# Performance work log

Hardware: AMD Instinct MI355X
Metric: run time of the kernel (lower is better)

The kernel has to match this reference:

```python
import jax, jax.numpy as jnp
import numpy as np

H, D = 2, 32          # heads, per-head dim
F = H * D             # hidden_channels = 64
IN = 128              # raw input feature dim
N_PAPER, N_AUTHOR = 200000, 100000
E = 400000            # edges per edge type


def setup_inputs() -> dict:
    ks = iter(jax.random.split(jax.random.key(0), 64))
    def nrm(shape, scale=1.0):
        return jax.random.normal(next(ks), shape, dtype=jnp.float32) * scale
    def rint(n, hi):
        return jax.random.randint(next(ks), (n,), 0, hi, dtype=jnp.int32)
    s_in = float(1.0 / np.sqrt(IN)); s_f = float(1.0 / np.sqrt(F)); s_d = float(1.0 / np.sqrt(D))
    return dict(
        x_paper=nrm((N_PAPER, IN)), x_author=nrm((N_AUTHOR, IN)),
        ei_writes_src=rint(E, N_AUTHOR), ei_writes_dst=rint(E, N_PAPER),
        ei_cites_src=rint(E, N_PAPER), ei_cites_dst=rint(E, N_PAPER),
        ei_rev_src=rint(E, N_PAPER), ei_rev_dst=rint(E, N_AUTHOR),
        lin_W_paper=nrm((IN, F), s_in), lin_b_paper=jnp.zeros((F,), jnp.float32),
        lin_W_author=nrm((IN, F), s_in), lin_b_author=jnp.zeros((F,), jnp.float32),
        kqv_W_paper=nrm((F, 3 * F), s_f), kqv_b_paper=jnp.zeros((3 * F,), jnp.float32),
        kqv_W_author=nrm((F, 3 * F), s_f), kqv_b_author=jnp.zeros((3 * F,), jnp.float32),
        a_W_paper=nrm((F, F), s_f), a_b_paper=jnp.zeros((F,), jnp.float32),
        a_W_author=nrm((F, F), s_f), a_b_author=jnp.zeros((F,), jnp.float32),
        skip_paper=jnp.ones((1,), jnp.float32), skip_author=jnp.ones((1,), jnp.float32),
        Wk_writes=nrm((H, D, D), s_d), Wv_writes=nrm((H, D, D), s_d), p_writes=jnp.ones((H,), jnp.float32),
        Wk_cites=nrm((H, D, D), s_d), Wv_cites=nrm((H, D, D), s_d), p_cites=jnp.ones((H,), jnp.float32),
        Wk_rev=nrm((H, D, D), s_d), Wv_rev=nrm((H, D, D), s_d), p_rev=jnp.ones((H,), jnp.float32),
        out_W=nrm((F, 1), s_f), out_b=jnp.zeros((1,), jnp.float32),
    )


def _seg_softmax(logits, seg, n):
    # softmax over edges grouped by destination node (PyG `softmax`)
    m = jax.ops.segment_max(logits, seg, num_segments=n)
    m = jnp.where(jnp.isfinite(m), m, 0.0)
    e = jnp.exp(logits - m[seg])
    s = jax.ops.segment_sum(e, seg, num_segments=n)
    return e / jnp.maximum(s[seg], 1e-16)


def _forward(x_paper, x_author,
             lin_W_paper, lin_b_paper, lin_W_author, lin_b_author,
             kqv_W_paper, kqv_b_paper, kqv_W_author, kqv_b_author,
             a_W_paper, a_b_paper, a_W_author, a_b_author,
             skip_paper, skip_author,
             Wk_writes, Wv_writes, p_writes,
             Wk_cites, Wv_cites, p_cites,
             Wk_rev, Wv_rev, p_rev,
             out_W, out_b,
             ei_writes_src, ei_writes_dst, ei_cites_src, ei_cites_dst,
             ei_rev_src, ei_rev_dst):
    # per-node-type input projection + relu
    xp = jax.nn.relu(x_paper @ lin_W_paper + lin_b_paper)      # [Np, F]
    xa = jax.nn.relu(x_author @ lin_W_author + lin_b_author)   # [Na, F]

    def kqv(x, W, b):
        k, q, v = jnp.split(x @ W + b, 3, axis=1)
        return k.reshape(-1, H, D), q.reshape(-1, H, D), v.reshape(-1, H, D)

    k_p, q_p, v_p = kqv(xp, kqv_W_paper, kqv_b_paper)
    k_a, q_a, v_a = kqv(xa, kqv_W_author, kqv_b_author)

    # global node indexing: paper nodes [0, Np), author nodes [Np, Np+Na)
    N = N_PAPER + N_AUTHOR
    q = jnp.concatenate([q_p, q_a], axis=0)  # [N, H, D]

    def rel(k_src, v_src, src, Wk, Wv):
        # per-edge-type, per-head relation transform of gathered source feats
        k = jnp.einsum('ehd,hdf->ehf', k_src[src], Wk)
        v = jnp.einsum('ehd,hdf->ehf', v_src[src], Wv)
        return k, v

    k1, v1 = rel(k_a, v_a, ei_writes_src, Wk_writes, Wv_writes)  # author->paper
    k2, v2 = rel(k_p, v_p, ei_cites_src, Wk_cites, Wv_cites)     # paper->paper
    k3, v3 = rel(k_p, v_p, ei_rev_src, Wk_rev, Wv_rev)           # paper->author

    k_e = jnp.concatenate([k1, k2, k3], axis=0)                  # [3E, H, D]
    v_e = jnp.concatenate([v1, v2, v3], axis=0)
    dst = jnp.concatenate([ei_writes_dst, ei_cites_dst, ei_rev_dst + N_PAPER], axis=0)
    p_e = jnp.concatenate([
        jnp.broadcast_to(p_writes, (E, H)),
        jnp.broadcast_to(p_cites, (E, H)),
        jnp.broadcast_to(p_rev, (E, H))], axis=0)                # [3E, H]

    logits = jnp.einsum('ehd,ehd->eh', q[dst], k_e) * p_e / jnp.sqrt(jnp.float32(D))
    attn = _seg_softmax(logits, dst, N)                          # [3E, H]
    agg = jax.ops.segment_sum(v_e * attn[..., None], dst, num_segments=N)
    agg = agg.reshape(N, F)
    out_p, out_a = agg[:N_PAPER], agg[N_PAPER:]

    gelu = lambda t: jax.nn.gelu(t, approximate=False)
    ap = gelu(out_p) @ a_W_paper + a_b_paper
    aa = gelu(out_a) @ a_W_author + a_b_author
    sp = jax.nn.sigmoid(skip_paper)
    sa = jax.nn.sigmoid(skip_author)
    hp = sp * ap + (1.0 - sp) * xp
    ha = sa * aa + (1.0 - sa) * xa  # computed by HGTConv; unused downstream (DCE'd)
    del ha
    return hp @ out_W + out_b       # [Np, 1]


def reference(x_paper, x_author, ei_writes_src, ei_writes_dst, ei_cites_src,
              ei_cites_dst, ei_rev_src, ei_rev_dst,
              lin_W_paper, lin_b_paper, lin_W_author, lin_b_author,
              kqv_W_paper, kqv_b_paper, kqv_W_author, kqv_b_author,
              a_W_paper, a_b_paper, a_W_author, a_b_author,
              skip_paper, skip_author,
              Wk_writes, Wv_writes, p_writes, Wk_cites, Wv_cites, p_cites,
              Wk_rev, Wv_rev, p_rev, out_W, out_b):
    return _forward(x_paper, x_author,
                    lin_W_paper, lin_b_paper, lin_W_author, lin_b_author,
                    kqv_W_paper, kqv_b_paper, kqv_W_author, kqv_b_author,
                    a_W_paper, a_b_paper, a_W_author, a_b_author,
                    skip_paper, skip_author,
                    Wk_writes, Wv_writes, p_writes,
                    Wk_cites, Wv_cites, p_cites,
                    Wk_rev, Wv_rev, p_rev,
                    out_W, out_b,
                    ei_writes_src, ei_writes_dst, ei_cites_src, ei_cites_dst,
                    ei_rev_src, ei_rev_dst)
```

## Files before the change

### kernel.cpp

```cpp
#include <hip/hip_runtime.h>

#define NP 200000
#define NA 100000
#define NE 400000
#define HH 2
#define DD 32
#define FF 64
#define INDIM 128

template <int FIN, int FOUT, bool RELU>
__global__ __launch_bounds__(256) void lin2_kernel(const float* __restrict__ X,
                                                   const float* __restrict__ W,
                                                   const float* __restrict__ b,
                                                   float* __restrict__ Y, int N) {
    constexpr int CT = FOUT / 64;
    constexpr int XP = FIN + 4;
    __shared__ float Ws[FIN * FOUT];
    __shared__ float Xs[64 * XP];
    for (int i = threadIdx.x; i < FIN * FOUT / 4; i += 256)
        ((float4*)Ws)[i] = ((const float4*)W)[i];
    const int ty = threadIdx.x >> 4;
    const int tx = threadIdx.x & 15;
    const int c0 = tx * 4;
    float4 breg[CT];
#pragma unroll
    for (int ct = 0; ct < CT; ++ct) breg[ct] = *(const float4*)(b + ct * 64 + c0);
    const int ntiles = (N + 63) >> 6;
    for (int tile = blockIdx.x; tile < ntiles; tile += gridDim.x) {
        const int base = tile << 6;
        __syncthreads();
        for (int i = threadIdx.x; i < 64 * FIN / 4; i += 256) {
            int r = i / (FIN / 4);
            int k4 = (i % (FIN / 4)) * 4;
            int row = base + r;
            if (row >= N) row = N - 1;
            *(float4*)(Xs + r * XP + k4) = *(const float4*)(X + (size_t)row * FIN + k4);
        }
        __syncthreads();
        float acc[4][4 * CT];
#pragma unroll
        for (int j = 0; j < 4; ++j)
#pragma unroll
            for (int ct = 0; ct < CT; ++ct) {
                acc[j][ct * 4 + 0] = breg[ct].x;
                acc[j][ct * 4 + 1] = breg[ct].y;
                acc[j][ct * 4 + 2] = breg[ct].z;
                acc[j][ct * 4 + 3] = breg[ct].w;
            }
        for (int k4 = 0; k4 < FIN; k4 += 4) {
            float4 xr[4];
#pragma unroll
            for (int j = 0; j < 4; ++j)
                xr[j] = *(const float4*)(Xs + (ty * 4 + j) * XP + k4);
            float4 wv[4][CT];
#pragma unroll
            for (int kk = 0; kk < 4; ++kk)
#pragma unroll
                for (int ct = 0; ct < CT; ++ct)
                    wv[kk][ct] = *(const float4*)(Ws + (k4 + kk) * FOUT + ct * 64 + c0);
#pragma unroll
            for (int kk = 0; kk < 4; ++kk) {
#pragma unroll
                for (int j = 0; j < 4; ++j) {
                    float xk[4] = {xr[j].x, xr[j].y, xr[j].z, xr[j].w};
                    float xv = xk[kk];
#pragma unroll
                    for (int ct = 0; ct < CT; ++ct) {
                        acc[j][ct * 4 + 0] = fmaf(xv, wv[kk][ct].x, acc[j][ct * 4 + 0]);
                        acc[j][ct * 4 + 1] = fmaf(xv, wv[kk][ct].y, acc[j][ct * 4 + 1]);
                        acc[j][ct * 4 + 2] = fmaf(xv, wv[kk][ct].z, acc[j][ct * 4 + 2]);
                        acc[j][ct * 4 + 3] = fmaf(xv, wv[kk][ct].w, acc[j][ct * 4 + 3]);
                    }
                }
            }
        }
#pragma unroll
        for (int j = 0; j < 4; ++j) {
            int row = base + ty * 4 + j;
            if (row < N) {
#pragma unroll
                for (int ct = 0; ct < CT; ++ct) {
                    float4 o;
                    o.x = acc[j][ct * 4 + 0]; o.y = acc[j][ct * 4 + 1];
                    o.z = acc[j][ct * 4 + 2]; o.w = acc[j][ct * 4 + 3];
                    if (RELU) {
                        o.x = fmaxf(o.x, 0.f); o.y = fmaxf(o.y, 0.f);
                        o.z = fmaxf(o.z, 0.f); o.w = fmaxf(o.w, 0.f);
                    }
                    *(float4*)(Y + (size_t)row * FOUT + ct * 64 + c0) = o;
                }
            }
        }
    }
}

__global__ void fold_paper(const float* __restrict__ kqvW, const float* __restrict__ kqvb,
                           const float* __restrict__ Wk, const float* __restrict__ Wv,
                           const float* __restrict__ p,
                           float* __restrict__ Wt, float* __restrict__ bt) {
    int c = blockIdx.x;
    int i = threadIdx.x;
    const float rsq = 0.1767766952966369f;
    if (c < 128) {
        int m = c >> 1, h = m >> 5, f = m & 31;
        bool isK = (c & 1) == 0;
        const float* M = isK ? Wk : Wv;
        float sc = isK ? p[h] * rsq : 1.f;
        int srcbase = (isK ? 0 : 128) + h * 32;
        float acc = 0.f;
        for (int d = 0; d < 32; ++d)
            acc += kqvW[i * 192 + srcbase + d] * M[(h * 32 + d) * 32 + f];
        Wt[i * 192 + c] = acc * sc;
        if (i == 0) {
            float bb = 0.f;
            for (int d = 0; d < 32; ++d)
                bb += kqvb[srcbase + d] * M[(h * 32 + d) * 32 + f];
            bt[c] = bb * sc;
        }
    } else {
        Wt[i * 192 + c] = kqvW[i * 192 + 64 + (c - 128)];
        if (i == 0) bt[c] = kqvb[64 + (c - 128)];
    }
}

__global__ void fold_author(const float* __restrict__ kqvW, const float* __restrict__ kqvb,
                            const float* __restrict__ Wk, const float* __restrict__ Wv,
                            const float* __restrict__ p,
                            float* __restrict__ Wt, float* __restrict__ bt) {
    int c = blockIdx.x;
    int i = threadIdx.x;
    const float rsq = 0.1767766952966369f;
    int m = c >> 1, h = m >> 5, f = m & 31;
    bool isK = (c & 1) == 0;
    const float* M = isK ? Wk : Wv;
    float sc = isK ? p[h] * rsq : 1.f;
    int srcbase = (isK ? 0 : 128) + h * 32;
    float acc = 0.f;
    for (int d = 0; d < 32; ++d)
        acc += kqvW[i * 192 + srcbase + d] * M[(h * 32 + d) * 32 + f];
    Wt[i * 128 + c] = acc * sc;
    if (i == 0) {
        float bb = 0.f;
        for (int d = 0; d < 32; ++d)
            bb += kqvb[srcbase + d] * M[(h * 32 + d) * 32 + f];
        bt[c] = bb * sc;
    }
}

__global__ void deg_count(const int* __restrict__ d1, const int* __restrict__ d2,
                          int* __restrict__ deg) {
    int i = blockIdx.x * blockDim.x + threadIdx.x;
    if (i < 2 * NE) {
        int d = (i < NE) ? d1[i] : d2[i - NE];
        atomicAdd(deg + d, 1);
    }
}

__device__ __forceinline__ int block_excl_scan_256(int v) {
    __shared__ int wsum[4];
    int lane = threadIdx.x & 63, wv = threadIdx.x >> 6;
    int incl = v;
#pragma unroll
    for (int off = 1; off < 64; off <<= 1) {
        int t = __shfl_up(incl, off, 64);
        if (lane >= off) incl += t;
    }
    if (lane == 63) wsum[wv] = incl;
    __syncthreads();
    int wo = 0;
#pragma unroll
    for (int k = 0; k < 4; ++k) wo += (k < wv) ? wsum[k] : 0;
    __syncthreads();
    return wo + incl - v;
}

__global__ void scan_bsum(const int* __restrict__ deg, int* __restrict__ bsum, int n) {
    __shared__ int wsum[4];
    int i = blockIdx.x * 256 + threadIdx.x;
    int v = (i < n) ? deg[i] : 0;
#pragma unroll
    for (int off = 32; off > 0; off >>= 1) v += __shfl_xor(v, off, 64);
    int lane = threadIdx.x & 63, wv = threadIdx.x >> 6;
    if (lane == 0) wsum[wv] = v;
    __syncthreads();
    if (threadIdx.x == 0) bsum[blockIdx.x] = wsum[0] + wsum[1] + wsum[2] + wsum[3];
}

__global__ void scan_mid(int* __restrict__ bsum, int nb) {
    __shared__ int carry;
    if (threadIdx.x == 0) carry = 0;
    __syncthreads();
    for (int base = 0; base < nb; base += 256) {
        int i = base + threadIdx.x;
        int v = (i < nb) ? bsum[i] : 0;
        int ex = block_excl_scan_256(v);
        int c = carry;
        __syncthreads();
        if (i < nb) bsum[i] = ex + c;
        if (threadIdx.x == 255) carry = c + ex + v;
        __syncthreads();
    }
}

__global__ void scan_final(const int* __restrict__ deg, const int* __restrict__ bsum,
                           int* __restrict__ row_ptr, int* __restrict__ cursor, int n) {
    int i = blockIdx.x * 256 + threadIdx.x;
    int v = (i < n) ? deg[i] : 0;
    int ex = block_excl_scan_256(v) + bsum[blockIdx.x];
    if (i < n) { row_ptr[i] = ex; cursor[i] = ex; }
}

__global__ void scatter_edges(const int* __restrict__ src, const int* __restrict__ dst,
                              int* __restrict__ cursor, int* __restrict__ payload, int relbit) {
    int e = blockIdx.x * blockDim.x + threadIdx.x;
    if (e < NE) {
        int d = dst[e];
        int pos = atomicAdd(cursor + d, 1);
        payload[pos] = src[e] | relbit;
    }
}

__global__ void csr_agg(const float* __restrict__ pG, const float* __restrict__ aG,
                        const int* __restrict__ row_ptr, const int* __restrict__ deg,
                        const int* __restrict__ payload, float* __restrict__ agg) {
    const int lane = threadIdx.x & 63;
    int wave_id = (blockIdx.x * blockDim.x + threadIdx.x) >> 6;
    int nwaves = (gridDim.x * blockDim.x) >> 6;
    for (int n = wave_id; n < NP; n += nwaves) {
        float q_l = pG[(size_t)n * 192 + 128 + lane];
        int start = row_ptr[n], dg = deg[n];
        float s = 0.f, acc = 0.f;
        for (int j = 0; j < dg; j += 4) {
            float kvx[4], vvy[4], msk[4];
#pragma unroll
            for (int c = 0; c < 4; ++c) {
                int jj = j + c;
                bool ok = jj < dg;
                int pl = payload[start + (ok ? jj : 0)];
                int rel = (int)((unsigned)pl >> 30);
                int sn = pl & 0x3FFFFFFF;
                const float* base = rel ? (pG + (size_t)sn * 192) : (aG + (size_t)sn * 128);
                float2 t = *(const float2*)(base + 2 * lane);
                kvx[c] = t.x;
                vvy[c] = t.y;
                msk[c] = ok ? 1.f : 0.f;
            }
#pragma unroll
            for (int c = 0; c < 4; ++c) {
                float prod = q_l * kvx[c];
#pragma unroll
                for (int off = 1; off < 32; off <<= 1) prod += __shfl_xor(prod, off, 64);
                float e = __expf(prod) * msk[c];
                s += e;
                acc = fmaf(e, vvy[c], acc);
            }
        }
        float inv = 1.f / fmaxf(s, 1e-16f);
        agg[(size_t)n * FF + lane] = acc * inv;
    }
}

__global__ __launch_bounds__(256) void finalize2(const float* __restrict__ agg,
                                                 const float* __restrict__ xp,
                                                 const float* __restrict__ aW,
                                                 const float* __restrict__ ab,
                                                 const float* __restrict__ skip,
                                                 const float* __restrict__ outW,
                                                 const float* __restrict__ outb,
                                                 float* __restrict__ out) {
    __shared__ float As[64 * 64];
    __shared__ float Gs[64 * 68];
    for (int i = threadIdx.x; i < 64 * 64 / 4; i += 256)
        ((float4*)As)[i] = ((const float4*)aW)[i];
    const int ty = threadIdx.x >> 4;
    const int tx = threadIdx.x & 15;
    const int c0 = tx * 4;
    const float sp = 1.f / (1.f + expf(-skip[0]));
    const float ob = outb[0];
    float4 ab4 = *(const float4*)(ab + c0);
    float4 oW4 = *(const float4*)(outW + c0);
    const int ntiles = NP >> 6;
    for (int tile = blockIdx.x; tile < ntiles; tile += gridDim.x) {
        const int base = tile << 6;
        __syncthreads();
        for (int i = threadIdx.x; i < 64 * 16; i += 256) {
            int r = i >> 4;
            int k4 = (i & 15) * 4;
            float4 v = *(const float4*)(agg + (size_t)(base + r) * 64 + k4);
            v.x = 0.5f * v.x * (1.f + erff(v.x * 0.7071067811865476f));
            v.y = 0.5f * v.y * (1.f + erff(v.y * 0.7071067811865476f));
            v.z = 0.5f * v.z * (1.f + erff(v.z * 0.7071067811865476f));
            v.w = 0.5f * v.w * (1.f + erff(v.w * 0.7071067811865476f));
            *(float4*)(Gs + r * 68 + k4) = v;
        }
        __syncthreads();
        float acc[4][4];
#pragma unroll
        for (int j = 0; j < 4; ++j) {
            acc[j][0] = ab4.x; acc[j][1] = ab4.y; acc[j][2] = ab4.z; acc[j][3] = ab4.w;
        }
        for (int k4 = 0; k4 < 64; k4 += 4) {
            float4 xr[4];
#pragma unroll
            for (int j = 0; j < 4; ++j)
                xr[j] = *(const float4*)(Gs + (ty * 4 + j) * 68 + k4);
            float4 wv[4];
#pragma unroll
            for (int kk = 0; kk < 4; ++kk)
                wv[kk] = *(const float4*)(As + (k4 + kk) * 64 + c0);
#pragma unroll
            for (int kk = 0; kk < 4; ++kk) {
#pragma unroll
                for (int j = 0; j < 4; ++j) {
                    float xk[4] = {xr[j].x, xr[j].y, xr[j].z, xr[j].w};
                    float xv = xk[kk];
                    acc[j][0] = fmaf(xv, wv[kk].x, acc[j][0]);
                    acc[j][1] = fmaf(xv, wv[kk].y, acc[j][1]);
                    acc[j][2] = fmaf(xv, wv[kk].z, acc[j][2]);
                    acc[j][3] = fmaf(xv, wv[kk].w, acc[j][3]);
                }
            }
        }
#pragma unroll
        for (int j = 0; j < 4; ++j) {
            int row = base + ty * 4 + j;
            float4 xv = *(const float4*)(xp + (size_t)row * 64 + c0);
            float t = (sp * acc[j][0] + (1.f - sp) * xv.x) * oW4.x;
            t = fmaf(sp * acc[j][1] + (1.f - sp) * xv.y, oW4.y, t);
            t = fmaf(sp * acc[j][2] + (1.f - sp) * xv.z, oW4.z, t);
            t = fmaf(sp * acc[j][3] + (1.f - sp) * xv.w, oW4.w, t);
#pragma unroll
            for (int off = 1; off < 16; off <<= 1) t += __shfl_xor(t, off, 64);
            if (tx == 0) out[row] = t + ob;
        }
    }
}

extern "C" void kernel_launch(void* const* d_in, const int* in_sizes, int n_in,
                              void* d_out, int out_size, void* d_ws, size_t ws_size,
                              hipStream_t stream) {
    const float* x_paper  = (const float*)d_in[0];
    const float* x_author = (const float*)d_in[1];
    const int*   w_src    = (const int*)d_in[2];
    const int*   w_dst    = (const int*)d_in[3];
    const int*   c_src    = (const int*)d_in[4];
    const int*   c_dst    = (const int*)d_in[5];
    const float* linWp = (const float*)d_in[8];
    const float* linbp = (const float*)d_in[9];
    const float* linWa = (const float*)d_in[10];
    const float* linba = (const float*)d_in[11];
    const float* kqvWp = (const float*)d_in[12];
    const float* kqvbp = (const float*)d_in[13];
    const float* kqvWa = (const float*)d_in[14];
    const float* kqvba = (const float*)d_in[15];
    const float* aWp   = (const float*)d_in[16];
    const float* abp   = (const float*)d_in[17];
    const float* skipp = (const float*)d_in[20];
    const float* Wk_w  = (const float*)d_in[22];
    const float* Wv_w  = (const float*)d_in[23];
    const float* p_w   = (const float*)d_in[24];
    const float* Wk_c  = (const float*)d_in[25];
    const float* Wv_c  = (const float*)d_in[26];
    const float* p_c   = (const float*)d_in[27];
    const float* outW  = (const float*)d_in[31];
    const float* outb  = (const float*)d_in[32];
    float* out = (float*)d_out;

    float* ws   = (float*)d_ws;
    float* xp   = ws;
    float* xa   = xp + (size_t)NP * FF;
    float* pG   = xa + (size_t)NA * FF;
    float* aG   = pG + (size_t)NP * 192;
    float* agg  = aG + (size_t)NA * 128;
    float* WtP  = agg + (size_t)NP * FF;
    float* btP  = WtP + 64 * 192;
    float* WtA  = btP + 192;
    float* btA  = WtA + 64 * 128;
    int* deg     = (int*)(btA + 128);
    int* row_ptr = deg + NP;
    int* cursor  = row_ptr + NP;
    int* bsum    = cursor + NP;
    int* payload = bsum + 1024;

    hipMemsetAsync(deg, 0, (size_t)NP * sizeof(int), stream);

    dim3 blk(256);
    const int NB = (NP + 255) / 256;

    fold_paper<<<192, 64, 0, stream>>>(kqvWp, kqvbp, Wk_c, Wv_c, p_c, WtP, btP);
    fold_author<<<128, 64, 0, stream>>>(kqvWa, kqvba, Wk_w, Wv_w, p_w, WtA, btA);

    lin2_kernel<INDIM, FF, true><<<1024, blk, 0, stream>>>(x_paper, linWp, linbp, xp, NP);
    lin2_kernel<INDIM, FF, true><<<1024, blk, 0, stream>>>(x_author, linWa, linba, xa, NA);
    lin2_kernel<FF, 192, false><<<1024, blk, 0, stream>>>(xp, WtP, btP, pG, NP);
    lin2_kernel<FF, 128, false><<<1024, blk, 0, stream>>>(xa, WtA, btA, aG, NA);

    deg_count<<<(2 * NE + 255) / 256, blk, 0, stream>>>(w_dst, c_dst, deg);
    scan_bsum<<<NB, blk, 0, stream>>>(deg, bsum, NP);
    scan_mid<<<1, blk, 0, stream>>>(bsum, NB);
    scan_final<<<NB, blk, 0, stream>>>(deg, bsum, row_ptr, cursor, NP);
    scatter_edges<<<(NE + 255) / 256, blk, 0, stream>>>(w_src, w_dst, cursor, payload, 0);
    scatter_edges<<<(NE + 255) / 256, blk, 0, stream>>>(c_src, c_dst, cursor, payload, 1 << 30);

    csr_agg<<<4096, blk, 0, stream>>>(pG, aG, row_ptr, deg, payload, agg);

    finalize2<<<1024, blk, 0, stream>>>(agg, xp, aWp, abp, skipp, outW, outb, out);
}
```

Before: 765.4 us.

## Merge independent prep kernels into block-partitioned megakernels and vectorize CSR gather

Independent stages (weight folding, input projections, degree counting; then KQV projections and block sums; then both edge scatters) are packed into single launches that split work by block index, reducing launch count and letting independent work overlap. The folded weight columns are interleaved so that each source row stores k and v for two features contiguously. This lets csr_agg load a float4 per lane and process two edges per wave-half, which shortens the shuffle reduction. The risks are uneven block partitioning inside the merged kernels and the larger shared-memory footprint that every block now reserves.

```diff
diff --git a/kernel.cpp b/kernel.cpp
--- a/kernel.cpp
+++ b/kernel.cpp
@@ -9,14 +9,13 @@
 #define INDIM 128
 
 template <int FIN, int FOUT, bool RELU>
-__global__ __launch_bounds__(256) void lin2_kernel(const float* __restrict__ X,
-                                                   const float* __restrict__ W,
-                                                   const float* __restrict__ b,
-                                                   float* __restrict__ Y, int N) {
+__device__ void lin2_dev(float* __restrict__ blob, const float* __restrict__ X,
+                         const float* __restrict__ W, const float* __restrict__ b,
+                         float* __restrict__ Y, int N, int bid, int nblocks) {
     constexpr int CT = FOUT / 64;
     constexpr int XP = FIN + 4;
-    __shared__ float Ws[FIN * FOUT];
-    __shared__ float Xs[64 * XP];
+    float* Ws = blob;
+    float* Xs = blob + FIN * FOUT;
     for (int i = threadIdx.x; i < FIN * FOUT / 4; i += 256)
         ((float4*)Ws)[i] = ((const float4*)W)[i];
     const int ty = threadIdx.x >> 4;
@@ -26,7 +25,7 @@
 #pragma unroll
     for (int ct = 0; ct < CT; ++ct) breg[ct] = *(const float4*)(b + ct * 64 + c0);
     const int ntiles = (N + 63) >> 6;
-    for (int tile = blockIdx.x; tile < ntiles; tile += gridDim.x) {
+    for (int tile = bid; tile < ntiles; tile += nblocks) {
         const int base = tile << 6;
         __syncthreads();
         for (int i = threadIdx.x; i < 64 * FIN / 4; i += 256) {
@@ -94,16 +93,17 @@
     }
 }
 
-__global__ void fold_paper(const float* __restrict__ kqvW, const float* __restrict__ kqvb,
-                           const float* __restrict__ Wk, const float* __restrict__ Wv,
-                           const float* __restrict__ p,
-                           float* __restrict__ Wt, float* __restrict__ bt) {
-    int c = blockIdx.x;
-    int i = threadIdx.x;
+__device__ void fold_paper_dev(const float* __restrict__ kqvW, const float* __restrict__ kqvb,
+                               const float* __restrict__ Wk, const float* __restrict__ Wv,
+                               const float* __restrict__ p,
+                               float* __restrict__ Wt, float* __restrict__ bt, int bid) {
+    int c = bid * 4 + (threadIdx.x >> 6);
+    int i = threadIdx.x & 63;
     const float rsq = 0.1767766952966369f;
     if (c < 128) {
-        int m = c >> 1, h = m >> 5, f = m & 31;
-        bool isK = (c & 1) == 0;
+        int pi = c >> 2, t = c & 3;
+        int h = pi >> 4, f = ((pi & 15) << 1) + (t >> 1);
+        bool isK = (t & 1) == 0;
         const float* M = isK ? Wk : Wv;
         float sc = isK ? p[h] * rsq : 1.f;
         int srcbase = (isK ? 0 : 128) + h * 32;
@@ -123,15 +123,16 @@
     }
 }
 
-__global__ void fold_author(const float* __restrict__ kqvW, const float* __restrict__ kqvb,
-                            const float* __restrict__ Wk, const float* __restrict__ Wv,
-                            const float* __restrict__ p,
-                            float* __restrict__ Wt, float* __restrict__ bt) {
-    int c = blockIdx.x;
-    int i = threadIdx.x;
+__device__ void fold_author_dev(const float* __restrict__ kqvW, const float* __restrict__ kqvb,
+                                const float* __restrict__ Wk, const float* __restrict__ Wv,
+                                const float* __restrict__ p,
+                                float* __restrict__ Wt, float* __restrict__ bt, int bid) {
+    int c = bid * 4 + (threadIdx.x >> 6);
+    int i = threadIdx.x & 63;
     const float rsq = 0.1767766952966369f;
-    int m = c >> 1, h = m >> 5, f = m & 31;
-    bool isK = (c & 1) == 0;
+    int pi = c >> 2, t = c & 3;
+    int h = pi >> 4, f = ((pi & 15) << 1) + (t >> 1);
+    bool isK = (t & 1) == 0;
     const float* M = isK ? Wk : Wv;
     float sc = isK ? p[h] * rsq : 1.f;
     int srcbase = (isK ? 0 : 128) + h * 32;
@@ -147,10 +148,10 @@
     }
 }
 
-__global__ void deg_count(const int* __restrict__ d1, const int* __restrict__ d2,
-                          int* __restrict__ deg) {
-    int i = blockIdx.x * blockDim.x + threadIdx.x;
-    if (i < 2 * NE) {
+__device__ void deg_count_dev(const int* __restrict__ d1, const int* __restrict__ d2,
+                              int* __restrict__ deg, int bid, int nblocks) {
+    int stride = nblocks * 256;
+    for (int i = bid * 256 + threadIdx.x; i < 2 * NE; i += stride) {
         int d = (i < NE) ? d1[i] : d2[i - NE];
         atomicAdd(deg + d, 1);
     }
@@ -174,16 +175,17 @@
     return wo + incl - v;
 }
 
-__global__ void scan_bsum(const int* __restrict__ deg, int* __restrict__ bsum, int n) {
+__device__ void scan_bsum_dev(const int* __restrict__ deg, int* __restrict__ bsum,
+                              int n, int bid) {
     __shared__ int wsum[4];
-    int i = blockIdx.x * 256 + threadIdx.x;
+    int i = bid * 256 + threadIdx.x;
     int v = (i < n) ? deg[i] : 0;
 #pragma unroll
     for (int off = 32; off > 0; off >>= 1) v += __shfl_xor(v, off, 64);
     int lane = threadIdx.x & 63, wv = threadIdx.x >> 6;
     if (lane == 0) wsum[wv] = v;
     __syncthreads();
-    if (threadIdx.x == 0) bsum[blockIdx.x] = wsum[0] + wsum[1] + wsum[2] + wsum[3];
+    if (threadIdx.x == 0) bsum[bid] = wsum[0] + wsum[1] + wsum[2] + wsum[3];
 }
 
 __global__ void scan_mid(int* __restrict__ bsum, int nb) {
@@ -210,9 +212,15 @@
     if (i < n) { row_ptr[i] = ex; cursor[i] = ex; }
 }
 
-__global__ void scatter_edges(const int* __restrict__ src, const int* __restrict__ dst,
-                              int* __restrict__ cursor, int* __restrict__ payload, int relbit) {
-    int e = blockIdx.x * blockDim.x + threadIdx.x;
+__global__ void mega_scatter(const int* __restrict__ w_src, const int* __restrict__ w_dst,
+                             const int* __restrict__ c_src, const int* __restrict__ c_dst,
+                             int* __restrict__ cursor, int* __restrict__ payload, int SB) {
+    int bid = blockIdx.x;
+    const int* src = (bid < SB) ? w_src : c_src;
+    const int* dst = (bid < SB) ? w_dst : c_dst;
+    int relbit = (bid < SB) ? 0 : (1 << 30);
+    int b = (bid < SB) ? bid : bid - SB;
+    int e = b * 256 + threadIdx.x;
     if (e < NE) {
         int d = dst[e];
         int pos = atomicAdd(cursor + d, 1);
@@ -220,43 +228,108 @@
     }
 }
 
+#define FOLD_P_B 48
+#define FOLD_A_B 32
+#define LIN_XP_B 512
+#define LIN_XA_B 256
+#define DEG_B 512
+#define MEGA1_B (FOLD_P_B + FOLD_A_B + LIN_XP_B + LIN_XA_B + DEG_B)
+
+__global__ __launch_bounds__(256) void mega1(
+    const float* x_paper, const float* x_author,
+    const float* linWp, const float* linbp, const float* linWa, const float* linba,
+    const float* kqvWp, const float* kqvbp, const float* kqvWa, const float* kqvba,
+    const float* Wk_w, const float* Wv_w, const float* p_w,
+    const float* Wk_c, const float* Wv_c, const float* p_c,
+    const int* w_dst, const int* c_dst,
+    float* xp, float* xa, float* WtP, float* btP, float* WtA, float* btA,
+    int* deg) {
+    __shared__ float blob[16640];
+    int bid = blockIdx.x;
+    if (bid < FOLD_P_B) {
+        fold_paper_dev(kqvWp, kqvbp, Wk_c, Wv_c, p_c, WtP, btP, bid);
+    } else if (bid < FOLD_P_B + FOLD_A_B) {
+        fold_author_dev(kqvWa, kqvba, Wk_w, Wv_w, p_w, WtA, btA, bid - FOLD_P_B);
+    } else if (bid < FOLD_P_B + FOLD_A_B + LIN_XP_B) {
+        lin2_dev<INDIM, FF, true>(blob, x_paper, linWp, linbp, xp, NP,
+                                  bid - (FOLD_P_B + FOLD_A_B), LIN_XP_B);
+    } else if (bid < FOLD_P_B + FOLD_A_B + LIN_XP_B + LIN_XA_B) {
+        lin2_dev<INDIM, FF, true>(blob, x_author, linWa, linba, xa, NA,
+                                  bid - (FOLD_P_B + FOLD_A_B + LIN_XP_B), LIN_XA_B);
+    } else {
+        deg_count_dev(w_dst, c_dst, deg, bid - (FOLD_P_B + FOLD_A_B + LIN_XP_B + LIN_XA_B), DEG_B);
+    }
+}
+
+#define LIN_PG_B 512
+#define LIN_AG_B 256
+#define NB_SCAN 782
+#define MEGA2_B (LIN_PG_B + LIN_AG_B + NB_SCAN)
+
+__global__ __launch_bounds__(256) void mega2(
+    const float* xp, const float* xa,
+    const float* WtP, const float* btP, const float* WtA, const float* btA,
+    float* pG, float* aG, const int* deg, int* bsum) {
+    __shared__ float blob[16640];
+    int bid = blockIdx.x;
+    if (bid < LIN_PG_B) {
+        lin2_dev<FF, 192, false>(blob, xp, WtP, btP, pG, NP, bid, LIN_PG_B);
+    } else if (bid < LIN_PG_B + LIN_AG_B) {
+        lin2_dev<FF, 128, false>(blob, xa, WtA, btA, aG, NA, bid - LIN_PG_B, LIN_AG_B);
+    } else {
+        scan_bsum_dev(deg, bsum, NP, bid - (LIN_PG_B + LIN_AG_B));
+    }
+}
+
 __global__ void csr_agg(const float* __restrict__ pG, const float* __restrict__ aG,
                         const int* __restrict__ row_ptr, const int* __restrict__ deg,
                         const int* __restrict__ payload, float* __restrict__ agg) {
     const int lane = threadIdx.x & 63;
+    const int pi = lane & 31;
+    const int half = lane >> 5;
+    const int h = pi >> 4;
+    const int f0 = (pi & 15) << 1;
     int wave_id = (blockIdx.x * blockDim.x + threadIdx.x) >> 6;
     int nwaves = (gridDim.x * blockDim.x) >> 6;
     for (int n = wave_id; n < NP; n += nwaves) {
-        float q_l = pG[(size_t)n * 192 + 128 + lane];
+        const float* qb = pG + (size_t)n * 192 + 128 + h * 32 + f0;
+        float2 q2 = *(const float2*)qb;
         int start = row_ptr[n], dg = deg[n];
-        float s = 0.f, acc = 0.f;
+        float s = 0.f;
+        float ax = 0.f, ay = 0.f;
         for (int j = 0; j < dg; j += 4) {
-            float kvx[4], vvy[4], msk[4];
-#pragma unroll
-            for (int c = 0; c < 4; ++c) {
-                int jj = j + c;
-                bool ok = jj < dg;
-                int pl = payload[start + (ok ? jj : 0)];
-                int rel = (int)((unsigned)pl >> 30);
-                int sn = pl & 0x3FFFFFFF;
-                const float* base = rel ? (pG + (size_t)sn * 192) : (aG + (size_t)sn * 128);
-                float2 t = *(const float2*)(base + 2 * lane);
-                kvx[c] = t.x;
-                vvy[c] = t.y;
-                msk[c] = ok ? 1.f : 0.f;
+            int jA = j + half;
+            int jB = j + 2 + half;
+            bool okA = jA < dg, okB = jB < dg;
+            int plA = payload[start + (okA ? jA : 0)];
+            int plB = payload[start + (okB ? jB : 0)];
+            int relA = (int)((unsigned)plA >> 30), relB = (int)((unsigned)plB >> 30);
+            int snA = plA & 0x3FFFFFFF, snB = plB & 0x3FFFFFFF;
+            const float* baseA = relA ? (pG + (size_t)snA * 192) : (aG + (size_t)snA * 128);
+            const float* baseB = relB ? (pG + (size_t)snB * 192) : (aG + (size_t)snB * 128);
+            float4 fA = *(const float4*)(baseA + 4 * pi);
+            float4 fB = *(const float4*)(baseB + 4 * pi);
+            float dA = q2.x * fA.x + q2.y * fA.z;
+            float dB = q2.x * fB.x + q2.y * fB.z;
+#pragma unroll
+            for (int off = 1; off < 16; off <<= 1) {
+                dA += __shfl_xor(dA, off, 64);
+                dB += __shfl_xor(dB, off, 64);
             }
-#pragma unroll
-            for (int c = 0; c < 4; ++c) {
-                float prod = q_l * kvx[c];
-#pragma unroll
-                for (int off = 1; off < 32; off <<= 1) prod += __shfl_xor(prod, off, 64);
-                float e = __expf(prod) * msk[c];
-                s += e;
-                acc = fmaf(e, vvy[c], acc);
-            }
-        }
-        float inv = 1.f / fmaxf(s, 1e-16f);
-        agg[(size_t)n * FF + lane] = acc * inv;
+            float eA = __expf(dA) * (okA ? 1.f : 0.f);
+            float eB = __expf(dB) * (okB ? 1.f : 0.f);
+            s += eA + eB;
+            ax = fmaf(eA, fA.y, ax); ax = fmaf(eB, fB.y, ax);
+            ay = fmaf(eA, fA.w, ay); ay = fmaf(eB, fB.w, ay);
+        }
+        s  += __shfl_xor(s, 32, 64);
+        ax += __shfl_xor(ax, 32, 64);
+        ay += __shfl_xor(ay, 32, 64);
+        if (half == 0) {
+            float inv = 1.f / fmaxf(s, 1e-16f);
+            float2 o; o.x = ax * inv; o.y = ay * inv;
+            *(float2*)(agg + (size_t)n * 64 + h * 32 + f0) = o;
+        }
     }
 }
 
@@ -385,22 +458,20 @@
     hipMemsetAsync(deg, 0, (size_t)NP * sizeof(int), stream);
 
     dim3 blk(256);
-    const int NB = (NP + 255) / 256;
-
-    fold_paper<<<192, 64, 0, stream>>>(kqvWp, kqvbp, Wk_c, Wv_c, p_c, WtP, btP);
-    fold_author<<<128, 64, 0, stream>>>(kqvWa, kqvba, Wk_w, Wv_w, p_w, WtA, btA);
-
-    lin2_kernel<INDIM, FF, true><<<1024, blk, 0, stream>>>(x_paper, linWp, linbp, xp, NP);
-    lin2_kernel<INDIM, FF, true><<<1024, blk, 0, stream>>>(x_author, linWa, linba, xa, NA);
-    lin2_kernel<FF, 192, false><<<1024, blk, 0, stream>>>(xp, WtP, btP, pG, NP);
-    lin2_kernel<FF, 128, false><<<1024, blk, 0, stream>>>(xa, WtA, btA, aG, NA);
-
-    deg_count<<<(2 * NE + 255) / 256, blk, 0, stream>>>(w_dst, c_dst, deg);
-    scan_bsum<<<NB, blk, 0, stream>>>(deg, bsum, NP);
-    scan_mid<<<1, blk, 0, stream>>>(bsum, NB);
-    scan_final<<<NB, blk, 0, stream>>>(deg, bsum, row_ptr, cursor, NP);
-    scatter_edges<<<(NE + 255) / 256, blk, 0, stream>>>(w_src, w_dst, cursor, payload, 0);
-    scatter_edges<<<(NE + 255) / 256, blk, 0, stream>>>(c_src, c_dst, cursor, payload, 1 << 30);
+    const int SB = (NE + 255) / 256;
+
+    mega1<<<MEGA1_B, blk, 0, stream>>>(x_paper, x_author, linWp, linbp, linWa, linba,
+                                       kqvWp, kqvbp, kqvWa, kqvba,
+                                       Wk_w, Wv_w, p_w, Wk_c, Wv_c, p_c,
+                                       w_dst, c_dst,
+                                       xp, xa, WtP, btP, WtA, btA, deg);
+
+    mega2<<<MEGA2_B, blk, 0, stream>>>(xp, xa, WtP, btP, WtA, btA, pG, aG, deg, bsum);
+
+    scan_mid<<<1, blk, 0, stream>>>(bsum, NB_SCAN);
+    scan_final<<<NB_SCAN, blk, 0, stream>>>(deg, bsum, row_ptr, cursor, NP);
+
+    mega_scatter<<<2 * SB, blk, 0, stream>>>(w_src, w_dst, c_src, c_dst, cursor, payload, SB);
 
     csr_agg<<<4096, blk, 0, stream>>>(pG, aG, row_ptr, deg, payload, agg);
 
```

After: 674.0 us. 11.9% less time.
